# Kernel optimization log

Measured on AMD Instinct MI355X. Metric: run time of the kernel, lower is better.

Reference implementation:

```python
import jax, jax.numpy as jnp
import numpy as np

D = 256; NH = 8; NL = 4; NP = 4; HD = D // NH
SHAPES = np.array([[64, 64], [32, 32], [16, 16], [8, 8]], dtype=np.int32)  # (H, W) per level
LSI = np.array([0, 4096, 5120, 5376], dtype=np.int32)
B = 4; LQ = int(SHAPES.prod(axis=1).sum())  # 5440


def setup_inputs() -> dict:
    key = jax.random.key(0)
    ks = jax.random.split(key, 16)
    p = lambda i, shape, s=0.02: jax.random.normal(ks[i], shape, dtype=jnp.float32) * s
    return dict(
        src=jax.random.normal(ks[0], (B, LQ, D), dtype=jnp.float32),
        pos=jax.random.normal(ks[1], (B, LQ, D), dtype=jnp.float32),
        reference_points=jax.random.uniform(ks[2], (B, LQ, NL, 2), dtype=jnp.float32),
        spatial_shapes=jnp.asarray(SHAPES),
        level_start_index=jnp.asarray(LSI),
        Wv=p(3, (D, D)), bv=jnp.zeros((D,), jnp.float32),
        Woff=p(4, (D, NH * NL * NP * 2)), boff=p(5, (NH * NL * NP * 2,)),
        Wattn=p(6, (D, NH * NL * NP)), battn=p(7, (NH * NL * NP,)),
        Wout=p(8, (D, D)), bout=jnp.zeros((D,), jnp.float32),
        g1=jnp.ones((D,), jnp.float32), b1=jnp.zeros((D,), jnp.float32),
        W1=p(9, (D, D)), bb1=jnp.zeros((D,), jnp.float32),
        W2=p(10, (D, D)), bb2=jnp.zeros((D,), jnp.float32),
        g3=jnp.ones((D,), jnp.float32), b3=jnp.zeros((D,), jnp.float32),
    )


def _ln(x, g, b, eps=1e-5):
    m = jnp.mean(x, -1, keepdims=True)
    v = jnp.mean(jnp.square(x - m), -1, keepdims=True)
    return (x - m) * jax.lax.rsqrt(v + eps) * g + b


def _bilinear(vflat, Hl, Wl, loc):
    # vflat: [B, Hl*Wl, nh, hd]; loc: [B, Lq, nh, np, 2] normalized to [0,1]
    # align_corners=False, zero padding (matches F.grid_sample in MSDeformAttn)
    x = loc[..., 0] * Wl - 0.5
    y = loc[..., 1] * Hl - 0.5
    x0 = jnp.floor(x); y0 = jnp.floor(y)
    fx = x - x0; fy = y - y0
    x0 = x0.astype(jnp.int32); y0 = y0.astype(jnp.int32)
    Bb, Lq, nh, npnt = x0.shape
    hd = vflat.shape[-1]
    out = jnp.zeros((Bb, Lq, nh, npnt, hd), vflat.dtype)
    for dy in (0, 1):
        for dx in (0, 1):
            xi = x0 + dx; yi = y0 + dy
            w = (fx if dx else 1.0 - fx) * (fy if dy else 1.0 - fy)
            valid = (xi >= 0) & (xi < Wl) & (yi >= 0) & (yi < Hl)
            idx = jnp.clip(yi, 0, Hl - 1) * Wl + jnp.clip(xi, 0, Wl - 1)  # [B,Lq,nh,np]
            idx = idx.transpose(0, 1, 3, 2).reshape(Bb, Lq * npnt, nh, 1)
            g = jnp.take_along_axis(vflat, idx, axis=1)
            g = g.reshape(Bb, Lq, npnt, nh, hd).transpose(0, 1, 3, 2, 4)
            out = out + g * (w * valid.astype(w.dtype))[..., None]
    return out  # [B, Lq, nh, np, hd]


def _forward(src, pos, reference_points, spatial_shapes, level_start_index,
             Wv, bv, Woff, boff, Wattn, battn, Wout, bout,
             g1, b1, W1, bb1, W2, bb2, g3, b3):
    shapes = np.asarray(spatial_shapes)
    lsi = np.asarray(level_start_index)
    Bq, Lq, Dm = src.shape
    q = src + pos  # with_pos_embed
    value = (src @ Wv + bv).reshape(Bq, Lq, NH, HD)
    off = (q @ Woff + boff).reshape(Bq, Lq, NH, NL, NP, 2)
    aw = jax.nn.softmax((q @ Wattn + battn).reshape(Bq, Lq, NH, NL * NP), axis=-1)
    aw = aw.reshape(Bq, Lq, NH, NL, NP)
    # offset normalizer is (W, H) per level
    norm = jnp.stack([shapes[:, 1].astype(np.float32), shapes[:, 0].astype(np.float32)], axis=-1)
    loc = reference_points[:, :, None, :, None, :] + off / norm[None, None, None, :, None, :]
    attended = jnp.zeros((Bq, Lq, NH, HD), src.dtype)
    for l in range(shapes.shape[0]):
        Hl, Wl = int(shapes[l, 0]), int(shapes[l, 1])
        s = int(lsi[l])
        vflat = value[:, s:s + Hl * Wl]
        sampled = _bilinear(vflat, Hl, Wl, loc[:, :, :, l])  # [B,Lq,nh,np,hd]
        attended = attended + jnp.einsum('blhpd,blhp->blhd', sampled, aw[:, :, :, l])
    src2 = attended.reshape(Bq, Lq, Dm) @ Wout + bout
    # residual + LayerNorm (dropout is identity in eval)
    sxy = _ln(src + src2, g1, b1)
    # FFN (d_ffn == d_model here), residual + LayerNorm
    h = jax.nn.relu(sxy @ W1 + bb1)
    return _ln(sxy + (h @ W2 + bb2), g3, b3)


def reference(src, pos, reference_points, spatial_shapes, level_start_index,
              Wv, bv, Woff, boff, Wattn, battn, Wout, bout,
              g1, b1, W1, bb1, W2, bb2, g3, b3):
    return _forward(src, pos, reference_points, spatial_shapes, level_start_index,
                    Wv, bv, Woff, boff, Wattn, battn, Wout, bout,
                    g1, b1, W1, bb1, W2, bb2, g3, b3)
```

## Files before the change

kernel.cpp:

```cpp
#include <hip/hip_runtime.h>
#include <cstddef>
#include <cstdint>

#define M_TOK 21760
#define LQ_ 5440

typedef _Float16 f16x8 __attribute__((ext_vector_type(8)));
typedef _Float16 h2v __attribute__((ext_vector_type(2)));
typedef float f32x4v __attribute__((ext_vector_type(4)));
typedef _Float16 half4v __attribute__((ext_vector_type(4)));

__device__ __forceinline__ unsigned short f2h(float f) {
  return __builtin_bit_cast(unsigned short, (_Float16)f);
}
__device__ __forceinline__ float h2f(unsigned short u) {
  return (float)__builtin_bit_cast(_Float16, u);
}

__global__ __launch_bounds__(256) void prep_k(
    const float* __restrict__ src, const float* __restrict__ pos,
    const float* __restrict__ Wv, const float* __restrict__ Woff,
    const float* __restrict__ Wattn, const float* __restrict__ Wout,
    const float* __restrict__ W1, const float* __restrict__ W2,
    unsigned short* __restrict__ s16, unsigned short* __restrict__ q16,
    unsigned short* __restrict__ G)
{
  const int b = blockIdx.x;
  if (b < 5440) {
    const int i = b * 256 + threadIdx.x;
    const float4 s = ((const float4*)src)[i];
    const float4 p = ((const float4*)pos)[i];
    ushort4 a, q;
    a.x = f2h(s.x); a.y = f2h(s.y); a.z = f2h(s.z); a.w = f2h(s.w);
    q.x = f2h(s.x + p.x); q.y = f2h(s.y + p.y); q.z = f2h(s.z + p.z); q.w = f2h(s.w + p.w);
    ((ushort4*)s16)[i] = a;
    ((ushort4*)q16)[i] = q;
  } else {
    const int gid = (b - 5440) * 256 + threadIdx.x;
    const float* srcs[6] = {Wv, Woff, Wattn, Wout, W1, W2};
    const int starts[7] = {0, 65536, 131072, 163840, 229376, 294912, 360448};
    const int Nn[6] = {256, 256, 128, 256, 256, 256};
    int m = 0;
#pragma unroll
    for (int i = 1; i < 6; ++i) m += (gid >= starts[i]);
    const int local = gid - starts[m];
    const int n = local >> 8;
    const int k = local & 255;
    G[gid] = f2h(srcs[m][(size_t)k * Nn[m] + n]);
  }
}

__global__ __launch_bounds__(256, 2) void gemm_qkv_k(
    const unsigned short* __restrict__ s16, const unsigned short* __restrict__ q16,
    const unsigned short* __restrict__ WvT, const unsigned short* __restrict__ WfT,
    const float* __restrict__ bv, const float* __restrict__ boff,
    const float* __restrict__ battn,
    unsigned short* __restrict__ value16, unsigned short* __restrict__ fused16)
{
  const int by = blockIdx.y;
  const bool isv = (by < 2);
  const unsigned short* A  = isv ? s16 : q16;
  const unsigned short* Wt = isv ? WvT : WfT;
  const int n0 = isv ? by * 128 : (by - 2) * 128;
  const int N  = isv ? 256 : 384;
  unsigned short* out16 = isv ? value16 : fused16;
  const float* bsel; int nsub;
  if (isv)            { bsel = bv;    nsub = 0; }
  else if (n0 < 256)  { bsel = boff;  nsub = 0; }
  else                { bsel = battn; nsub = 256; }

  __shared__ unsigned short As[128 * 64];
  __shared__ unsigned short Bs[128 * 64];
  const int t = threadIdx.x;
  const int lane = t & 63, wave = t >> 6;
  const int wm = wave >> 1, wn = wave & 1;
  const int m0 = blockIdx.x * 128;

  const int lrow = lane >> 3;
  const int pcol = (lane & 7) << 4;
  const int scol = pcol ^ (lrow << 4);

  f32x4v acc[4][4];
#pragma unroll
  for (int i = 0; i < 4; ++i)
#pragma unroll
    for (int j = 0; j < 4; ++j) acc[i][j] = (f32x4v){0.f, 0.f, 0.f, 0.f};

  const int fr = lane & 15;
  const int fkb = (lane >> 4) << 4;

  for (int k0 = 0; k0 < 256; k0 += 64) {
#pragma unroll
    for (int i = 0; i < 4; ++i) {
      const int row = wave * 32 + i * 8 + lrow;
      const unsigned short* g = A + (size_t)(m0 + row) * 256 + k0 + (scol >> 1);
      unsigned short* s = As + (wave * 32 + i * 8) * 64;
      __builtin_amdgcn_global_load_lds(
          (const __attribute__((address_space(1))) void*)g,
          (__attribute__((address_space(3))) void*)s, 16, 0, 0);
    }
#pragma unroll
    for (int i = 0; i < 4; ++i) {
      const int row = wave * 32 + i * 8 + lrow;
      const unsigned short* g = Wt + (size_t)(n0 + row) * 256 + k0 + (scol >> 1);
      unsigned short* s = Bs + (wave * 32 + i * 8) * 64;
      __builtin_amdgcn_global_load_lds(
          (const __attribute__((address_space(1))) void*)g,
          (__attribute__((address_space(3))) void*)s, 16, 0, 0);
    }
    __syncthreads();

    f16x8 af[4][2], bfr[4][2];
#pragma unroll
    for (int i = 0; i < 4; ++i) {
      const int row = wm * 64 + i * 16 + fr;
      const char* base = (const char*)As + row * 128;
#pragma unroll
      for (int kk = 0; kk < 2; ++kk)
        af[i][kk] = *(const f16x8*)(base + ((kk * 64 + fkb) ^ ((row & 7) << 4)));
    }
#pragma unroll
    for (int j = 0; j < 4; ++j) {
      const int row = wn * 64 + j * 16 + fr;
      const char* base = (const char*)Bs + row * 128;
#pragma unroll
      for (int kk = 0; kk < 2; ++kk)
        bfr[j][kk] = *(const f16x8*)(base + ((kk * 64 + fkb) ^ ((row & 7) << 4)));
    }
#pragma unroll
    for (int i = 0; i < 4; ++i)
#pragma unroll
      for (int j = 0; j < 4; ++j) {
        acc[i][j] = __builtin_amdgcn_mfma_f32_16x16x32_f16(af[i][0], bfr[j][0], acc[i][j], 0, 0, 0);
        acc[i][j] = __builtin_amdgcn_mfma_f32_16x16x32_f16(af[i][1], bfr[j][1], acc[i][j], 0, 0, 0);
      }
    __syncthreads();
  }

  const int fq = lane >> 4;
#pragma unroll
  for (int j = 0; j < 4; ++j) {
    const int n = n0 + wn * 64 + j * 16 + fr;
    const float bj = bsel[n - nsub];
#pragma unroll
    for (int i = 0; i < 4; ++i) {
#pragma unroll
      for (int r = 0; r < 4; ++r) {
        const int m = m0 + wm * 64 + i * 16 + fq * 4 + r;
        out16[(size_t)m * N + n] = f2h(acc[i][j][r] + bj);
      }
    }
  }
}

__global__ __launch_bounds__(256, 2) void gemm16_k(
    const unsigned short* __restrict__ A, const unsigned short* __restrict__ Wt,
    const float* __restrict__ bias, unsigned short* __restrict__ out16,
    int N, int relu)
{
  __shared__ unsigned short As[128 * 64];
  __shared__ unsigned short Bs[128 * 64];
  const int t = threadIdx.x;
  const int lane = t & 63, wave = t >> 6;
  const int wm = wave >> 1, wn = wave & 1;
  const int m0 = blockIdx.x * 128, n0 = blockIdx.y * 128;

  const int lrow = lane >> 3;
  const int pcol = (lane & 7) << 4;
  const int scol = pcol ^ (lrow << 4);

  f32x4v acc[4][4];
#pragma unroll
  for (int i = 0; i < 4; ++i)
#pragma unroll
    for (int j = 0; j < 4; ++j) acc[i][j] = (f32x4v){0.f, 0.f, 0.f, 0.f};

  const int fr = lane & 15;
  const int fkb = (lane >> 4) << 4;

  for (int k0 = 0; k0 < 256; k0 += 64) {
#pragma unroll
    for (int i = 0; i < 4; ++i) {
      const int row = wave * 32 + i * 8 + lrow;
      const unsigned short* g = A + (size_t)(m0 + row) * 256 + k0 + (scol >> 1);
      unsigned short* s = As + (wave * 32 + i * 8) * 64;
      __builtin_amdgcn_global_load_lds(
          (const __attribute__((address_space(1))) void*)g,
          (__attribute__((address_space(3))) void*)s, 16, 0, 0);
    }
#pragma unroll
    for (int i = 0; i < 4; ++i) {
      const int row = wave * 32 + i * 8 + lrow;
      const unsigned short* g = Wt + (size_t)(n0 + row) * 256 + k0 + (scol >> 1);
      unsigned short* s = Bs + (wave * 32 + i * 8) * 64;
      __builtin_amdgcn_global_load_lds(
          (const __attribute__((address_space(1))) void*)g,
          (__attribute__((address_space(3))) void*)s, 16, 0, 0);
    }
    __syncthreads();

    f16x8 af[4][2], bfr[4][2];
#pragma unroll
    for (int i = 0; i < 4; ++i) {
      const int row = wm * 64 + i * 16 + fr;
      const char* base = (const char*)As + row * 128;
#pragma unroll
      for (int kk = 0; kk < 2; ++kk)
        af[i][kk] = *(const f16x8*)(base + ((kk * 64 + fkb) ^ ((row & 7) << 4)));
    }
#pragma unroll
    for (int j = 0; j < 4; ++j) {
      const int row = wn * 64 + j * 16 + fr;
      const char* base = (const char*)Bs + row * 128;
#pragma unroll
      for (int kk = 0; kk < 2; ++kk)
        bfr[j][kk] = *(const f16x8*)(base + ((kk * 64 + fkb) ^ ((row & 7) << 4)));
    }
#pragma unroll
    for (int i = 0; i < 4; ++i)
#pragma unroll
      for (int j = 0; j < 4; ++j) {
        acc[i][j] = __builtin_amdgcn_mfma_f32_16x16x32_f16(af[i][0], bfr[j][0], acc[i][j], 0, 0, 0);
        acc[i][j] = __builtin_amdgcn_mfma_f32_16x16x32_f16(af[i][1], bfr[j][1], acc[i][j], 0, 0, 0);
      }
    __syncthreads();
  }

  const int fq = lane >> 4;
#pragma unroll
  for (int j = 0; j < 4; ++j) {
    const int n = n0 + wn * 64 + j * 16 + fr;
    const float bj = bias[n];
#pragma unroll
    for (int i = 0; i < 4; ++i) {
#pragma unroll
      for (int r = 0; r < 4; ++r) {
        const int m = m0 + wm * 64 + i * 16 + fq * 4 + r;
        float v = acc[i][j][r] + bj;
        if (relu) v = fmaxf(v, 0.f);
        out16[(size_t)m * N + n] = f2h(v);
      }
    }
  }
}

__global__ __launch_bounds__(512, 4) void gemm_ln_k(
    const unsigned short* __restrict__ A, const unsigned short* __restrict__ Wt,
    const float* __restrict__ bias, const float* __restrict__ resf,
    const unsigned short* __restrict__ res16,
    const float* __restrict__ g, const float* __restrict__ b,
    float* __restrict__ outf, unsigned short* __restrict__ out16)
{
  __shared__ unsigned short As[32 * 64];
  __shared__ unsigned short Bs[256 * 64 + 288];
  const int t = threadIdx.x;
  const int lane = t & 63, wave = t >> 6;
  const int rt = wave & 1, cg = wave >> 1;
  const int m0 = blockIdx.x * 32;

  const int lrow = lane >> 3;
  const int pcol = (lane & 7) << 4;
  const int scol = pcol ^ (lrow << 4);

  f32x4v acc[4];
#pragma unroll
  for (int j = 0; j < 4; ++j) acc[j] = (f32x4v){0.f, 0.f, 0.f, 0.f};

  const int fr = lane & 15;
  const int fq = lane >> 4;
  const int fkb = fq << 4;

  for (int k0 = 0; k0 < 256; k0 += 64) {
    if (wave < 4) {
      const int row = wave * 8 + lrow;
      const unsigned short* gp = A + (size_t)(m0 + row) * 256 + k0 + (scol >> 1);
      unsigned short* s = As + (wave * 8) * 64;
      __builtin_amdgcn_global_load_lds(
          (const __attribute__((address_space(1))) void*)gp,
          (__attribute__((address_space(3))) void*)s, 16, 0, 0);
    }
#pragma unroll
    for (int i = 0; i < 4; ++i) {
      const int row = wave * 32 + i * 8 + lrow;
      const unsigned short* gp = Wt + (size_t)row * 256 + k0 + (scol >> 1);
      unsigned short* s = Bs + (wave * 32 + i * 8) * 64;
      __builtin_amdgcn_global_load_lds(
          (const __attribute__((address_space(1))) void*)gp,
          (__attribute__((address_space(3))) void*)s, 16, 0, 0);
    }
    __syncthreads();

    f16x8 af0, af1;
    {
      const int arow = rt * 16 + fr;
      const char* abase = (const char*)As + arow * 128;
      af0 = *(const f16x8*)(abase + ((0 + fkb) ^ ((arow & 7) << 4)));
      af1 = *(const f16x8*)(abase + ((64 + fkb) ^ ((arow & 7) << 4)));
    }
#pragma unroll
    for (int j = 0; j < 4; ++j) {
      const int brow = cg * 64 + j * 16 + fr;
      const char* bbase = (const char*)Bs + brow * 128;
      const f16x8 b0 = *(const f16x8*)(bbase + ((0 + fkb) ^ ((brow & 7) << 4)));
      const f16x8 b1 = *(const f16x8*)(bbase + ((64 + fkb) ^ ((brow & 7) << 4)));
      acc[j] = __builtin_amdgcn_mfma_f32_16x16x32_f16(af0, b0, acc[j], 0, 0, 0);
      acc[j] = __builtin_amdgcn_mfma_f32_16x16x32_f16(af1, b1, acc[j], 0, 0, 0);
    }
    __syncthreads();
  }

  float* Cs = (float*)Bs;
#pragma unroll
  for (int j = 0; j < 4; ++j) {
    const int col = cg * 64 + j * 16 + fr;
#pragma unroll
    for (int rr = 0; rr < 4; ++rr) {
      const int row = rt * 16 + fq * 4 + rr;
      Cs[row * 260 + col] = acc[j][rr];
    }
  }
  __syncthreads();

  const int lg = lane >> 4, li = lane & 15;
  const int row = wave * 4 + lg;
  const size_t rowoff = (size_t)(m0 + row) * 256;

  float4 v[4];
  float s = 0.f;
#pragma unroll
  for (int c4 = 0; c4 < 4; ++c4) {
    const int col = c4 * 64 + li * 4;
    float4 x = *(float4*)&Cs[row * 260 + col];
    const float4 bi = *(const float4*)&bias[col];
    float4 rv;
    if (resf) {
      rv = *(const float4*)&resf[rowoff + col];
    } else {
      const ushort4 r16 = *(const ushort4*)&res16[rowoff + col];
      rv.x = h2f(r16.x); rv.y = h2f(r16.y); rv.z = h2f(r16.z); rv.w = h2f(r16.w);
    }
    x.x += bi.x + rv.x; x.y += bi.y + rv.y;
    x.z += bi.z + rv.z; x.w += bi.w + rv.w;
    v[c4] = x;
    s += x.x + x.y + x.z + x.w;
  }
#pragma unroll
  for (int o = 1; o < 16; o <<= 1) s += __shfl_xor(s, o);
  const float mean = s * (1.f / 256.f);
  float ss = 0.f;
#pragma unroll
  for (int c4 = 0; c4 < 4; ++c4) {
    const float d0 = v[c4].x - mean, d1 = v[c4].y - mean;
    const float d2 = v[c4].z - mean, d3 = v[c4].w - mean;
    ss += d0 * d0 + d1 * d1 + d2 * d2 + d3 * d3;
  }
#pragma unroll
  for (int o = 1; o < 16; o <<= 1) ss += __shfl_xor(ss, o);
  const float rstd = rsqrtf(ss * (1.f / 256.f) + 1e-5f);

#pragma unroll
  for (int c4 = 0; c4 < 4; ++c4) {
    const int col = c4 * 64 + li * 4;
    const float4 gv = *(const float4*)&g[col];
    const float4 bv = *(const float4*)&b[col];
    float4 o4;
    o4.x = (v[c4].x - mean) * rstd * gv.x + bv.x;
    o4.y = (v[c4].y - mean) * rstd * gv.y + bv.y;
    o4.z = (v[c4].z - mean) * rstd * gv.z + bv.z;
    o4.w = (v[c4].w - mean) * rstd * gv.w + bv.w;
    if (outf) *(float4*)(outf + rowoff + col) = o4;
    if (out16) {
      ushort4 o;
      o.x = f2h(o4.x); o.y = f2h(o4.y); o.z = f2h(o4.z); o.w = f2h(o4.w);
      *(ushort4*)(out16 + rowoff + col) = o;
    }
  }
}

__global__ __launch_bounds__(256) void samp_k(
    const unsigned short* __restrict__ value16, const unsigned short* __restrict__ fused16,
    const float* __restrict__ ref, unsigned short* __restrict__ att16)
{
  const int b = blockIdx.x;
  const int wg = (b & 7) * 340 + (b >> 3);
  const int tok0 = wg * 8;

  __shared__ half4v swv[8][136];
  __shared__ uint2  siv[8][136];
  const int t = threadIdx.x;
  const _Float16* fh = (const _Float16*)fused16;

#pragma unroll
  for (int it = 0; it < 4; ++it) {
    const int idx = it * 256 + t;
    const int ti = idx >> 7;
    const int e  = idx & 127;
    const int tok = tok0 + ti;
    const int h = e >> 4;
    const int lvl = (e >> 2) & 3;
    const int HW[4] = {64, 32, 16, 8};
    const int LS[4] = {0, 4096, 5120, 5376};
    const int Wl = HW[lvl];

    const float lg = (float)fh[(size_t)tok * 384 + 256 + e];
    float mx = lg;
#pragma unroll
    for (int o = 1; o < 16; o <<= 1) mx = fmaxf(mx, __shfl_xor(mx, o, 16));
    const float ex = __expf(lg - mx);
    float sm = ex;
#pragma unroll
    for (int o = 1; o < 16; o <<= 1) sm += __shfl_xor(sm, o, 16);
    const float a = ex / sm;

    const float ox = (float)fh[(size_t)tok * 384 + e * 2 + 0];
    const float oy = (float)fh[(size_t)tok * 384 + e * 2 + 1];
    const float rx = ref[(size_t)tok * 8 + lvl * 2 + 0];
    const float ry = ref[(size_t)tok * 8 + lvl * 2 + 1];
    const float x = rx * (float)Wl + ox - 0.5f;
    const float y = ry * (float)Wl + oy - 0.5f;
    const float x0f = floorf(x), y0f = floorf(y);
    const float fx = x - x0f, fy = y - y0f;
    const int x0 = (int)x0f, y0 = (int)y0f;

    const int xi1 = x0 + 1, yi1 = y0 + 1;
    const float wx0 = 1.f - fx, wx1 = fx, wy0 = 1.f - fy, wy1 = fy;
    const int xc0 = min(max(x0, 0), Wl - 1), xc1 = min(max(xi1, 0), Wl - 1);
    const int yc0 = min(max(y0, 0), Wl - 1), yc1 = min(max(yi1, 0), Wl - 1);
    const bool vx0 = (x0 >= 0) & (x0 < Wl), vx1 = (xi1 >= 0) & (xi1 < Wl);
    const bool vy0 = (y0 >= 0) & (y0 < Wl), vy1 = (yi1 >= 0) & (yi1 < Wl);
    half4v hw;
    hw.x = (_Float16)((vx0 & vy0) ? a * wx0 * wy0 : 0.f);
    hw.y = (_Float16)((vx1 & vy0) ? a * wx1 * wy0 : 0.f);
    hw.z = (_Float16)((vx0 & vy1) ? a * wx0 * wy1 : 0.f);
    hw.w = (_Float16)((vx1 & vy1) ? a * wx1 * wy1 : 0.f);
    const unsigned i00 = (unsigned)(LS[lvl] + yc0 * Wl + xc0);
    const unsigned i01 = (unsigned)(LS[lvl] + yc0 * Wl + xc1);
    const unsigned i10 = (unsigned)(LS[lvl] + yc1 * Wl + xc0);
    const unsigned i11 = (unsigned)(LS[lvl] + yc1 * Wl + xc1);
    uint2 io;
    io.x = i00 | (i01 << 16);
    io.y = i10 | (i11 << 16);
    const int sl = e + h;
    swv[ti][sl] = hw;
    siv[ti][sl] = io;
  }
  __syncthreads();

  const int wave = t >> 6, lane = t & 63;
  const int ti = wave * 2 + (lane >> 5);
  const int h = (lane >> 2) & 7, dg = lane & 3;
  const int tok = tok0 + ti;
  const int vbase = (tok0 / LQ_) * LQ_;
  const char* vb = (const char*)(value16 + (size_t)vbase * 256);
  const int laneoff = h * 64 + dg * 16;
  h2v a0 = {0, 0}, a1 = {0, 0}, a2 = {0, 0}, a3 = {0, 0};
  const int ebase = h * 17;

#pragma unroll 4
  for (int p = 0; p < 16; ++p) {
    const half4v hw = swv[ti][ebase + p];
    const uint2 io = siv[ti][ebase + p];
    const int o00 = (int)((io.x & 0xFFFFu) << 9) + laneoff;
    const int o01 = (int)((io.x >> 16) << 9) + laneoff;
    const int o10 = (int)((io.y & 0xFFFFu) << 9) + laneoff;
    const int o11 = (int)((io.y >> 16) << 9) + laneoff;
    const uint4 u0 = *(const uint4*)(vb + o00);
    const uint4 u1 = *(const uint4*)(vb + o01);
    const uint4 u2 = *(const uint4*)(vb + o10);
    const uint4 u3 = *(const uint4*)(vb + o11);
#define CORNER(U, WI) {                                            \
    const h2v w2 = __builtin_shufflevector(hw, hw, WI, WI);        \
    a0 += w2 * __builtin_bit_cast(h2v, U.x);                       \
    a1 += w2 * __builtin_bit_cast(h2v, U.y);                       \
    a2 += w2 * __builtin_bit_cast(h2v, U.z);                       \
    a3 += w2 * __builtin_bit_cast(h2v, U.w); }
    CORNER(u0, 0) CORNER(u1, 1) CORNER(u2, 2) CORNER(u3, 3)
#undef CORNER
  }

  uint4 o;
  o.x = __builtin_bit_cast(unsigned, a0);
  o.y = __builtin_bit_cast(unsigned, a1);
  o.z = __builtin_bit_cast(unsigned, a2);
  o.w = __builtin_bit_cast(unsigned, a3);
  *(uint4*)(att16 + (size_t)tok * 256 + h * 32 + dg * 8) = o;
}

extern "C" void kernel_launch(void* const* d_in, const int* in_sizes, int n_in,
                              void* d_out, int out_size, void* d_ws, size_t ws_size,
                              hipStream_t stream)
{
  const float* src   = (const float*)d_in[0];
  const float* pos   = (const float*)d_in[1];
  const float* ref   = (const float*)d_in[2];
  const float* Wv    = (const float*)d_in[5];
  const float* bv    = (const float*)d_in[6];
  const float* Woff  = (const float*)d_in[7];
  const float* boff  = (const float*)d_in[8];
  const float* Wattn = (const float*)d_in[9];
  const float* battn = (const float*)d_in[10];
  const float* Wout  = (const float*)d_in[11];
  const float* bout  = (const float*)d_in[12];
  const float* g1    = (const float*)d_in[13];
  const float* b1    = (const float*)d_in[14];
  const float* W1    = (const float*)d_in[15];
  const float* bb1   = (const float*)d_in[16];
  const float* W2    = (const float*)d_in[17];
  const float* bb2   = (const float*)d_in[18];
  const float* g3    = (const float*)d_in[19];
  const float* b3    = (const float*)d_in[20];

  float* out = (float*)d_out;
  char* ws = (char*)d_ws;
  const size_t M = M_TOK;

  unsigned short* value16 = (unsigned short*)ws;
  unsigned short* fused16 = (unsigned short*)(ws + M * 256 * 4);
  unsigned short* bufE = fused16 + M * 384;
  unsigned short* bufF = bufE + M * 256;
  unsigned short* bufG = bufF + M * 256;

  unsigned short* WvT     = bufG + 0;
  unsigned short* WfusedT = bufG + 65536;
  unsigned short* WoutT   = bufG + 163840;
  unsigned short* W1T     = bufG + 229376;
  unsigned short* W2T     = bufG + 294912;

  const dim3 blk(256);

  prep_k<<<dim3(6848), blk, 0, stream>>>(src, pos, Wv, Woff, Wattn, Wout, W1, W2,
                                         bufE, bufF, bufG);
  gemm_qkv_k<<<dim3(170, 5), blk, 0, stream>>>(bufE, bufF, WvT, WfusedT,
                                               bv, boff, battn, value16, fused16);
  samp_k<<<dim3(2720), blk, 0, stream>>>(value16, fused16, ref, bufE);
  gemm_ln_k<<<dim3(680), dim3(512), 0, stream>>>(bufE, WoutT, bout, src, nullptr,
                                                 g1, b1, nullptr, bufF);
  gemm16_k<<<dim3(170, 2), blk, 0, stream>>>(bufF, W1T, bb1, bufE, 256, 1);
  gemm_ln_k<<<dim3(680), dim3(512), 0, stream>>>(bufE, W2T, bb2, nullptr, bufF,
                                                 g3, b3, out, nullptr);
}
```

Measured before the change: 101.3 us.

## Fuse FFN GEMMs with LayerNorm and remap QKV GEMM blocks across XCDs

Measured after the change: 99.54 us. About the same (-1.7%).

```diff
diff --git a/kernel.cpp b/kernel.cpp
--- a/kernel.cpp
+++ b/kernel.cpp
@@ -57,7 +57,13 @@
     const float* __restrict__ battn,
     unsigned short* __restrict__ value16, unsigned short* __restrict__ fused16)
 {
-  const int by = blockIdx.y;
+  const int id = blockIdx.x;
+  const int xcd = id & 7;
+  const int local = id >> 3;
+  const int sid = xcd * 106 + min(xcd, 2) + local;
+  const int bx = sid / 5;
+  const int by = sid % 5;
+
   const bool isv = (by < 2);
   const unsigned short* A  = isv ? s16 : q16;
   const unsigned short* Wt = isv ? WvT : WfT;
@@ -74,7 +80,7 @@
   const int t = threadIdx.x;
   const int lane = t & 63, wave = t >> 6;
   const int wm = wave >> 1, wn = wave & 1;
-  const int m0 = blockIdx.x * 128;
+  const int m0 = bx * 128;
 
   const int lrow = lane >> 3;
   const int pcol = (lane & 7) << 4;
@@ -148,97 +154,6 @@
       for (int r = 0; r < 4; ++r) {
         const int m = m0 + wm * 64 + i * 16 + fq * 4 + r;
         out16[(size_t)m * N + n] = f2h(acc[i][j][r] + bj);
-      }
-    }
-  }
-}
-
-__global__ __launch_bounds__(256, 2) void gemm16_k(
-    const unsigned short* __restrict__ A, const unsigned short* __restrict__ Wt,
-    const float* __restrict__ bias, unsigned short* __restrict__ out16,
-    int N, int relu)
-{
-  __shared__ unsigned short As[128 * 64];
-  __shared__ unsigned short Bs[128 * 64];
-  const int t = threadIdx.x;
-  const int lane = t & 63, wave = t >> 6;
-  const int wm = wave >> 1, wn = wave & 1;
-  const int m0 = blockIdx.x * 128, n0 = blockIdx.y * 128;
-
-  const int lrow = lane >> 3;
-  const int pcol = (lane & 7) << 4;
-  const int scol = pcol ^ (lrow << 4);
-
-  f32x4v acc[4][4];
-#pragma unroll
-  for (int i = 0; i < 4; ++i)
-#pragma unroll
-    for (int j = 0; j < 4; ++j) acc[i][j] = (f32x4v){0.f, 0.f, 0.f, 0.f};
-
-  const int fr = lane & 15;
-  const int fkb = (lane >> 4) << 4;
-
-  for (int k0 = 0; k0 < 256; k0 += 64) {
-#pragma unroll
-    for (int i = 0; i < 4; ++i) {
-      const int row = wave * 32 + i * 8 + lrow;
-      const unsigned short* g = A + (size_t)(m0 + row) * 256 + k0 + (scol >> 1);
-      unsigned short* s = As + (wave * 32 + i * 8) * 64;
-      __builtin_amdgcn_global_load_lds(
-          (const __attribute__((address_space(1))) void*)g,
-          (__attribute__((address_space(3))) void*)s, 16, 0, 0);
-    }
-#pragma unroll
-    for (int i = 0; i < 4; ++i) {
-      const int row = wave * 32 + i * 8 + lrow;
-      const unsigned short* g = Wt + (size_t)(n0 + row) * 256 + k0 + (scol >> 1);
-      unsigned short* s = Bs + (wave * 32 + i * 8) * 64;
-      __builtin_amdgcn_global_load_lds(
-          (const __attribute__((address_space(1))) void*)g,
-          (__attribute__((address_space(3))) void*)s, 16, 0, 0);
-    }
-    __syncthreads();
-
-    f16x8 af[4][2], bfr[4][2];
-#pragma unroll
-    for (int i = 0; i < 4; ++i) {
-      const int row = wm * 64 + i * 16 + fr;
-      const char* base = (const char*)As + row * 128;
-#pragma unroll
-      for (int kk = 0; kk < 2; ++kk)
-        af[i][kk] = *(const f16x8*)(base + ((kk * 64 + fkb) ^ ((row & 7) << 4)));
-    }
-#pragma unroll
-    for (int j = 0; j < 4; ++j) {
-      const int row = wn * 64 + j * 16 + fr;
-      const char* base = (const char*)Bs + row * 128;
-#pragma unroll
-      for (int kk = 0; kk < 2; ++kk)
-        bfr[j][kk] = *(const f16x8*)(base + ((kk * 64 + fkb) ^ ((row & 7) << 4)));
-    }
-#pragma unroll
-    for (int i = 0; i < 4; ++i)
-#pragma unroll
-      for (int j = 0; j < 4; ++j) {
-        acc[i][j] = __builtin_amdgcn_mfma_f32_16x16x32_f16(af[i][0], bfr[j][0], acc[i][j], 0, 0, 0);
-        acc[i][j] = __builtin_amdgcn_mfma_f32_16x16x32_f16(af[i][1], bfr[j][1], acc[i][j], 0, 0, 0);
-      }
-    __syncthreads();
-  }
-
-  const int fq = lane >> 4;
-#pragma unroll
-  for (int j = 0; j < 4; ++j) {
-    const int n = n0 + wn * 64 + j * 16 + fr;
-    const float bj = bias[n];
-#pragma unroll
-    for (int i = 0; i < 4; ++i) {
-#pragma unroll
-      for (int r = 0; r < 4; ++r) {
-        const int m = m0 + wm * 64 + i * 16 + fq * 4 + r;
-        float v = acc[i][j][r] + bj;
-        if (relu) v = fmaxf(v, 0.f);
-        out16[(size_t)m * N + n] = f2h(v);
       }
     }
   }
@@ -374,6 +289,158 @@
       o.x = f2h(o4.x); o.y = f2h(o4.y); o.z = f2h(o4.z); o.w = f2h(o4.w);
       *(ushort4*)(out16 + rowoff + col) = o;
     }
+  }
+}
+
+__global__ __launch_bounds__(512, 4) void gemm_ffn_ln_k(
+    const unsigned short* __restrict__ sxy16,
+    const unsigned short* __restrict__ W1T, const unsigned short* __restrict__ W2T,
+    const float* __restrict__ bb1, const float* __restrict__ bb2,
+    const float* __restrict__ g, const float* __restrict__ b,
+    float* __restrict__ outf)
+{
+  __shared__ unsigned short Bs[256 * 64 + 288];
+  __shared__ unsigned short Hs[32 * 264];
+  const int t = threadIdx.x;
+  const int lane = t & 63, wave = t >> 6;
+  const int rt = wave & 1, cg = wave >> 1;
+  const int m0 = blockIdx.x * 32;
+
+  const int lrow = lane >> 3;
+  const int pcol = (lane & 7) << 4;
+  const int scol = pcol ^ (lrow << 4);
+
+  const int fr = lane & 15;
+  const int fq = lane >> 4;
+  const int fkb = fq << 4;
+
+  f32x4v acc[4];
+#pragma unroll
+  for (int j = 0; j < 4; ++j) acc[j] = (f32x4v){0.f, 0.f, 0.f, 0.f};
+
+  for (int k0 = 0; k0 < 256; k0 += 64) {
+#pragma unroll
+    for (int i = 0; i < 4; ++i) {
+      const int row = wave * 32 + i * 8 + lrow;
+      const unsigned short* gp = W1T + (size_t)row * 256 + k0 + (scol >> 1);
+      unsigned short* s = Bs + (wave * 32 + i * 8) * 64;
+      __builtin_amdgcn_global_load_lds(
+          (const __attribute__((address_space(1))) void*)gp,
+          (__attribute__((address_space(3))) void*)s, 16, 0, 0);
+    }
+    const unsigned short* ap = sxy16 + (size_t)(m0 + rt * 16 + fr) * 256 + k0 + fq * 8;
+    const f16x8 af0 = *(const f16x8*)ap;
+    const f16x8 af1 = *(const f16x8*)(ap + 32);
+    __syncthreads();
+#pragma unroll
+    for (int j = 0; j < 4; ++j) {
+      const int brow = cg * 64 + j * 16 + fr;
+      const char* bbase = (const char*)Bs + brow * 128;
+      const f16x8 b0 = *(const f16x8*)(bbase + ((0 + fkb) ^ ((brow & 7) << 4)));
+      const f16x8 b1 = *(const f16x8*)(bbase + ((64 + fkb) ^ ((brow & 7) << 4)));
+      acc[j] = __builtin_amdgcn_mfma_f32_16x16x32_f16(af0, b0, acc[j], 0, 0, 0);
+      acc[j] = __builtin_amdgcn_mfma_f32_16x16x32_f16(af1, b1, acc[j], 0, 0, 0);
+    }
+    __syncthreads();
+  }
+
+  {
+    float b1j[4];
+#pragma unroll
+    for (int j = 0; j < 4; ++j) b1j[j] = bb1[cg * 64 + j * 16 + fr];
+#pragma unroll
+    for (int j = 0; j < 4; ++j) {
+      const int col = cg * 64 + j * 16 + fr;
+#pragma unroll
+      for (int rr = 0; rr < 4; ++rr) {
+        const int row = rt * 16 + fq * 4 + rr;
+        Hs[row * 264 + col] = f2h(fmaxf(acc[j][rr] + b1j[j], 0.f));
+      }
+      acc[j] = (f32x4v){0.f, 0.f, 0.f, 0.f};
+    }
+  }
+  __syncthreads();
+
+  for (int k0 = 0; k0 < 256; k0 += 64) {
+#pragma unroll
+    for (int i = 0; i < 4; ++i) {
+      const int row = wave * 32 + i * 8 + lrow;
+      const unsigned short* gp = W2T + (size_t)row * 256 + k0 + (scol >> 1);
+      unsigned short* s = Bs + (wave * 32 + i * 8) * 64;
+      __builtin_amdgcn_global_load_lds(
+          (const __attribute__((address_space(1))) void*)gp,
+          (__attribute__((address_space(3))) void*)s, 16, 0, 0);
+    }
+    const int arow = rt * 16 + fr;
+    const f16x8 af0 = *(const f16x8*)&Hs[arow * 264 + k0 + fq * 8];
+    const f16x8 af1 = *(const f16x8*)&Hs[arow * 264 + k0 + fq * 8 + 32];
+    __syncthreads();
+#pragma unroll
+    for (int j = 0; j < 4; ++j) {
+      const int brow = cg * 64 + j * 16 + fr;
+      const char* bbase = (const char*)Bs + brow * 128;
+      const f16x8 b0 = *(const f16x8*)(bbase + ((0 + fkb) ^ ((brow & 7) << 4)));
+      const f16x8 b1 = *(const f16x8*)(bbase + ((64 + fkb) ^ ((brow & 7) << 4)));
+      acc[j] = __builtin_amdgcn_mfma_f32_16x16x32_f16(af0, b0, acc[j], 0, 0, 0);
+      acc[j] = __builtin_amdgcn_mfma_f32_16x16x32_f16(af1, b1, acc[j], 0, 0, 0);
+    }
+    __syncthreads();
+  }
+
+  float* Cs = (float*)Bs;
+#pragma unroll
+  for (int j = 0; j < 4; ++j) {
+    const int col = cg * 64 + j * 16 + fr;
+#pragma unroll
+    for (int rr = 0; rr < 4; ++rr) {
+      const int row = rt * 16 + fq * 4 + rr;
+      Cs[row * 260 + col] = acc[j][rr];
+    }
+  }
+  __syncthreads();
+
+  const int lg = lane >> 4, li = lane & 15;
+  const int row = wave * 4 + lg;
+  const size_t rowoff = (size_t)(m0 + row) * 256;
+
+  float4 v[4];
+  float s = 0.f;
+#pragma unroll
+  for (int c4 = 0; c4 < 4; ++c4) {
+    const int col = c4 * 64 + li * 4;
+    float4 x = *(float4*)&Cs[row * 260 + col];
+    const float4 bi = *(const float4*)&bb2[col];
+    const ushort4 r16 = *(const ushort4*)&sxy16[rowoff + col];
+    x.x += bi.x + h2f(r16.x); x.y += bi.y + h2f(r16.y);
+    x.z += bi.z + h2f(r16.z); x.w += bi.w + h2f(r16.w);
+    v[c4] = x;
+    s += x.x + x.y + x.z + x.w;
+  }
+#pragma unroll
+  for (int o = 1; o < 16; o <<= 1) s += __shfl_xor(s, o);
+  const float mean = s * (1.f / 256.f);
+  float ss = 0.f;
+#pragma unroll
+  for (int c4 = 0; c4 < 4; ++c4) {
+    const float d0 = v[c4].x - mean, d1 = v[c4].y - mean;
+    const float d2 = v[c4].z - mean, d3 = v[c4].w - mean;
+    ss += d0 * d0 + d1 * d1 + d2 * d2 + d3 * d3;
+  }
+#pragma unroll
+  for (int o = 1; o < 16; o <<= 1) ss += __shfl_xor(ss, o);
+  const float rstd = rsqrtf(ss * (1.f / 256.f) + 1e-5f);
+
+#pragma unroll
+  for (int c4 = 0; c4 < 4; ++c4) {
+    const int col = c4 * 64 + li * 4;
+    const float4 gv = *(const float4*)&g[col];
+    const float4 bv = *(const float4*)&b[col];
+    float4 o4;
+    o4.x = (v[c4].x - mean) * rstd * gv.x + bv.x;
+    o4.y = (v[c4].y - mean) * rstd * gv.y + bv.y;
+    o4.z = (v[c4].z - mean) * rstd * gv.z + bv.z;
+    o4.w = (v[c4].w - mean) * rstd * gv.w + bv.w;
+    *(float4*)(outf + rowoff + col) = o4;
   }
 }
 
@@ -530,12 +597,11 @@
 
   prep_k<<<dim3(6848), blk, 0, stream>>>(src, pos, Wv, Woff, Wattn, Wout, W1, W2,
                                          bufE, bufF, bufG);
-  gemm_qkv_k<<<dim3(170, 5), blk, 0, stream>>>(bufE, bufF, WvT, WfusedT,
-                                               bv, boff, battn, value16, fused16);
+  gemm_qkv_k<<<dim3(850), blk, 0, stream>>>(bufE, bufF, WvT, WfusedT,
+                                            bv, boff, battn, value16, fused16);
   samp_k<<<dim3(2720), blk, 0, stream>>>(value16, fused16, ref, bufE);
   gemm_ln_k<<<dim3(680), dim3(512), 0, stream>>>(bufE, WoutT, bout, src, nullptr,
                                                  g1, b1, nullptr, bufF);
-  gemm16_k<<<dim3(170, 2), blk, 0, stream>>>(bufF, W1T, bb1, bufE, 256, 1);
-  gemm_ln_k<<<dim3(680), dim3(512), 0, stream>>>(bufE, W2T, bb2, nullptr, bufF,
-                                                 g3, b3, out, nullptr);
-}
+  gemm_ffn_ln_k<<<dim3(680), dim3(512), 0, stream>>>(bufF, W1T, W2T, bb1, bb2,
+                                                     g3, b3, out);
+}
```
